# Optimization experiments

Hardware: AMD Instinct MI355X
Metric: run time of the kernel (lower is better)

Reference implementation:

```python
import jax, jax.numpy as jnp
import numpy as np

D_K = 64

def setup_inputs() -> dict:
    key = jax.random.key(0)
    kq, kk, kv, km = jax.random.split(key, 4)
    B, H, S, D = 8, 12, 1024, D_K
    Q = jax.random.normal(kq, (B, H, S, D), dtype=jnp.float32)
    K = jax.random.normal(kk, (B, H, S, D), dtype=jnp.float32)
    V = jax.random.normal(kv, (B, H, S, D), dtype=jnp.float32)
    # boolean mask: True = masked out (as used by masked_fill_)
    attn_mask = jax.random.randint(km, (B, H, S, S), 0, 2) == 1
    return {"Q": Q, "K": K, "V": V, "attn_mask": attn_mask}

def reference(Q, K, V, attn_mask):
    # scores: [B, H, S, S]
    scale = 1.0 / np.sqrt(D_K).astype(np.float32)
    scores = jnp.einsum('bhqd,bhkd->bhqk', Q, K) * scale
    scores = jnp.where(attn_mask, jnp.float32(-1e9), scores)
    attn = jax.nn.softmax(scores, axis=-1)
    context = jnp.einsum('bhqk,bhkd->bhqd', attn, V)
    return (context, attn)
```

## Files before the change

### kernel.cpp

```cpp
#include <hip/hip_runtime.h>

#define S_LEN  1024
#define D_KK   64
#define N_HEAD 96

#define TK 256
#define BQ 16

__global__ __launch_bounds__(256, 2) void attn_softmax_kernel(
    const float* __restrict__ Qg, const float* __restrict__ Kg,
    const int* __restrict__ maskg, float* __restrict__ attng)
{
    __shared__ float kt[D_KK][TK + 1];
    __shared__ float qs[BQ][68];

    const int t    = threadIdx.x;
    const int lane = t & 63;
    const int wave = t >> 6;
    const int head = blockIdx.y;
    const int q0   = blockIdx.x * BQ;
    const int rbase = wave << 2;

    {
        const int r  = t >> 4;
        const int d0 = (t & 15) << 2;
        const float4 qv = *(const float4*)(Qg + ((size_t)head * S_LEN + q0 + r) * D_KK + d0);
        qs[r][d0 + 0] = qv.x; qs[r][d0 + 1] = qv.y;
        qs[r][d0 + 2] = qv.z; qs[r][d0 + 3] = qv.w;
    }

    float s[4][16];

    for (int kt_i = 0; kt_i < S_LEN / TK; ++kt_i) {
        __syncthreads();
        {
            const int d0 = (t & 15) << 2;
            const int kb = t >> 4;
            #pragma unroll
            for (int c = 0; c < TK / 16; ++c) {
                const int kl = c * 16 + kb;
                const float4 kv = *(const float4*)(Kg + ((size_t)head * S_LEN + kt_i * TK + kl) * D_KK + d0);
                kt[d0 + 0][kl] = kv.x;
                kt[d0 + 1][kl] = kv.y;
                kt[d0 + 2][kl] = kv.z;
                kt[d0 + 3][kl] = kv.w;
            }
        }
        __syncthreads();

        float acc[4][4] = {{0.f,0.f,0.f,0.f},{0.f,0.f,0.f,0.f},
                           {0.f,0.f,0.f,0.f},{0.f,0.f,0.f,0.f}};
        for (int d0 = 0; d0 < D_KK; d0 += 4) {
            float4 qv[4];
            #pragma unroll
            for (int r = 0; r < 4; ++r)
                qv[r] = *(const float4*)(&qs[rbase + r][d0]);
            #pragma unroll
            for (int dd = 0; dd < 4; ++dd) {
                float kv[4];
                #pragma unroll
                for (int j = 0; j < 4; ++j)
                    kv[j] = kt[d0 + dd][lane + 64 * j];
                #pragma unroll
                for (int r = 0; r < 4; ++r) {
                    const float qd = (&qv[r].x)[dd];
                    #pragma unroll
                    for (int j = 0; j < 4; ++j)
                        acc[r][j] = fmaf(qd, kv[j], acc[r][j]);
                }
            }
        }
        #pragma unroll
        for (int r = 0; r < 4; ++r)
            #pragma unroll
            for (int j = 0; j < 4; ++j)
                s[r][kt_i * 4 + j] = acc[r][j] * 0.125f;
    }

    #pragma unroll
    for (int r = 0; r < 4; ++r) {
        const int q = q0 + rbase + r;
        const int*  mrow = maskg + ((size_t)head * S_LEN + q) * S_LEN;
        float*      arow = attng + ((size_t)head * S_LEN + q) * S_LEN;
        float m = -3.0e38f;
        #pragma unroll
        for (int j = 0; j < 16; ++j) {
            if (mrow[lane + 64 * j]) s[r][j] = -1.0e9f;
            m = fmaxf(m, s[r][j]);
        }
        #pragma unroll
        for (int off = 32; off >= 1; off >>= 1)
            m = fmaxf(m, __shfl_xor(m, off, 64));
        float l = 0.0f;
        #pragma unroll
        for (int j = 0; j < 16; ++j) {
            s[r][j] = __expf(s[r][j] - m);
            l += s[r][j];
        }
        #pragma unroll
        for (int off = 32; off >= 1; off >>= 1)
            l += __shfl_xor(l, off, 64);
        const float inv = 1.0f / l;
        #pragma unroll
        for (int j = 0; j < 16; ++j)
            arow[lane + 64 * j] = s[r][j] * inv;
    }
}

#define TKB 128

__global__ __launch_bounds__(256, 2) void attn_pv_kernel(
    const float* __restrict__ attng, const float* __restrict__ Vg,
    float* __restrict__ ctxg)
{
    __shared__ float at[64][132];
    __shared__ float vt[TKB][68];

    const int t    = threadIdx.x;
    const int tx   = t & 15;
    const int ty   = t >> 4;
    const int head = blockIdx.y;
    const int q0   = blockIdx.x * 64;

    float acc[4][4] = {{0.f,0.f,0.f,0.f},{0.f,0.f,0.f,0.f},
                       {0.f,0.f,0.f,0.f},{0.f,0.f,0.f,0.f}};

    for (int k0 = 0; k0 < S_LEN; k0 += TKB) {
        __syncthreads();
        #pragma unroll
        for (int p = 0; p < 8; ++p) {
            const int i  = t + 256 * p;
            const int q  = i >> 5;
            const int kk = (i & 31) << 2;
            const float4 a = *(const float4*)(attng + ((size_t)head * S_LEN + q0 + q) * S_LEN + k0 + kk);
            *(float4*)(&at[q][kk]) = a;
        }
        #pragma unroll
        for (int p = 0; p < 8; ++p) {
            const int i  = t + 256 * p;
            const int k  = i >> 4;
            const int d0 = (i & 15) << 2;
            const float4 v = *(const float4*)(Vg + ((size_t)head * S_LEN + k0 + k) * D_KK + d0);
            *(float4*)(&vt[k][d0]) = v;
        }
        __syncthreads();

        for (int k = 0; k < TKB; ++k) {
            const float4 v = *(const float4*)(&vt[k][tx << 2]);
            #pragma unroll
            for (int qq = 0; qq < 4; ++qq) {
                const float a = at[(ty << 2) + qq][k];
                acc[qq][0] = fmaf(a, v.x, acc[qq][0]);
                acc[qq][1] = fmaf(a, v.y, acc[qq][1]);
                acc[qq][2] = fmaf(a, v.z, acc[qq][2]);
                acc[qq][3] = fmaf(a, v.w, acc[qq][3]);
            }
        }
    }

    #pragma unroll
    for (int qq = 0; qq < 4; ++qq) {
        float4 o;
        o.x = acc[qq][0]; o.y = acc[qq][1]; o.z = acc[qq][2]; o.w = acc[qq][3];
        *(float4*)(ctxg + ((size_t)head * S_LEN + q0 + (ty << 2) + qq) * D_KK + (tx << 2)) = o;
    }
}

extern "C" void kernel_launch(void* const* d_in, const int* in_sizes, int n_in,
                              void* d_out, int out_size, void* d_ws, size_t ws_size,
                              hipStream_t stream) {
    const float* Q    = (const float*)d_in[0];
    const float* K    = (const float*)d_in[1];
    const float* V    = (const float*)d_in[2];
    const int*   mask = (const int*)d_in[3];

    float* ctx  = (float*)d_out;
    float* attn = ctx + (size_t)N_HEAD * S_LEN * D_KK;

    dim3 gridA(S_LEN / BQ, N_HEAD);
    attn_softmax_kernel<<<gridA, 256, 0, stream>>>(Q, K, mask, attn);

    dim3 gridB(S_LEN / 64, N_HEAD);
    attn_pv_kernel<<<gridB, 256, 0, stream>>>(attn, V, ctx);
}
```

Baseline: 1.041 ms.

## Fuse QK softmax and PV into one bf16 MFMA kernel

Replaces the two fp32 SIMT kernels with a single kernel that converts Q, K and V to bf16 and computes QK^T and PV with 16x16x32 bf16 MFMA instructions. Unnormalized exponentials are kept packed in registers, row sums are reduced, and the normalized probabilities are written to the attention output and reused directly for the PV product. This avoids re-reading the attention matrix from global memory. The softmax drops max subtraction, which risks overflow for large scores, and bf16 rounding lowers precision of both outputs. Holding 128 registers of packed probabilities per thread may also limit occupancy.

```diff
diff --git a/kernel.cpp b/kernel.cpp
--- a/kernel.cpp
+++ b/kernel.cpp
@@ -4,166 +4,169 @@
 #define D_KK   64
 #define N_HEAD 96
 
-#define TK 256
-#define BQ 16
+typedef float f32x4 __attribute__((ext_vector_type(4)));
+typedef short bf16x8 __attribute__((ext_vector_type(8)));
+typedef short bf16x4 __attribute__((ext_vector_type(4)));
 
-__global__ __launch_bounds__(256, 2) void attn_softmax_kernel(
+__device__ __forceinline__ unsigned short f2bf(float f) {
+    union { float f; unsigned u; } v; v.f = f;
+    unsigned r = v.u + 0x7fffu + ((v.u >> 16) & 1u);
+    return (unsigned short)(r >> 16);
+}
+__device__ __forceinline__ float bf2f(unsigned short b) {
+    union { float f; unsigned u; } v; v.u = ((unsigned)b) << 16;
+    return v.f;
+}
+
+__global__ __launch_bounds__(256, 2) void fused_attn_kernel(
     const float* __restrict__ Qg, const float* __restrict__ Kg,
-    const int* __restrict__ maskg, float* __restrict__ attng)
+    const float* __restrict__ Vg, const int* __restrict__ maskg,
+    float* __restrict__ ctxg, float* __restrict__ attng)
 {
-    __shared__ float kt[D_KK][TK + 1];
-    __shared__ float qs[BQ][68];
+    __shared__ short qs[64][72];
+    __shared__ short ks[128][72];
+    __shared__ short vt[64][136];
+    __shared__ short ps[64][136];
 
     const int t    = threadIdx.x;
     const int lane = t & 63;
     const int wave = t >> 6;
+    const int quad = lane >> 4;
+    const int l16  = lane & 15;
     const int head = blockIdx.y;
-    const int q0   = blockIdx.x * BQ;
-    const int rbase = wave << 2;
+    const int q0   = blockIdx.x * 64;
 
-    {
-        const int r  = t >> 4;
-        const int d0 = (t & 15) << 2;
-        const float4 qv = *(const float4*)(Qg + ((size_t)head * S_LEN + q0 + r) * D_KK + d0);
-        qs[r][d0 + 0] = qv.x; qs[r][d0 + 1] = qv.y;
-        qs[r][d0 + 2] = qv.z; qs[r][d0 + 3] = qv.w;
+    const size_t headQ = (size_t)head * S_LEN * D_KK;
+    const float* Qh = Qg + headQ + (size_t)q0 * D_KK;
+    const float* Kh = Kg + headQ;
+    const float* Vh = Vg + headQ;
+    const int*   mh = maskg + ((size_t)head * S_LEN + q0) * S_LEN;
+    float*       ah = attng + ((size_t)head * S_LEN + q0) * S_LEN;
+    float*       ch = ctxg + headQ + (size_t)q0 * D_KK;
+
+    #pragma unroll
+    for (int p = 0; p < 4; ++p) {
+        const int i = t + 256 * p;
+        const int row = i >> 4, c4 = (i & 15) << 2;
+        const f32x4 qv = *(const f32x4*)(Qh + (size_t)row * D_KK + c4);
+        bf16x4 qb;
+        qb[0] = (short)f2bf(qv[0]); qb[1] = (short)f2bf(qv[1]);
+        qb[2] = (short)f2bf(qv[2]); qb[3] = (short)f2bf(qv[3]);
+        *(bf16x4*)(&qs[row][c4]) = qb;
     }
+    __syncthreads();
 
-    float s[4][16];
+    bf16x8 aq[2];
+    #pragma unroll
+    for (int d0 = 0; d0 < 2; ++d0)
+        aq[d0] = *(const bf16x8*)(&qs[16 * wave + l16][d0 * 32 + quad * 8]);
 
-    for (int kt_i = 0; kt_i < S_LEN / TK; ++kt_i) {
+    unsigned pk[128];
+    float lsum[4] = {0.f, 0.f, 0.f, 0.f};
+
+    #pragma unroll
+    for (int kt = 0; kt < 8; ++kt) {
+        #pragma unroll
+        for (int p = 0; p < 8; ++p) {
+            const int i = t + 256 * p;
+            const int row = i >> 4, c4 = (i & 15) << 2;
+            const f32x4 kv = *(const f32x4*)(Kh + (size_t)(kt * 128 + row) * D_KK + c4);
+            bf16x4 kb;
+            kb[0] = (short)f2bf(kv[0]); kb[1] = (short)f2bf(kv[1]);
+            kb[2] = (short)f2bf(kv[2]); kb[3] = (short)f2bf(kv[3]);
+            *(bf16x4*)(&ks[row][c4]) = kb;
+        }
         __syncthreads();
-        {
-            const int d0 = (t & 15) << 2;
-            const int kb = t >> 4;
+
+        #pragma unroll
+        for (int ct = 0; ct < 8; ++ct) {
+            f32x4 c = {0.f, 0.f, 0.f, 0.f};
             #pragma unroll
-            for (int c = 0; c < TK / 16; ++c) {
-                const int kl = c * 16 + kb;
-                const float4 kv = *(const float4*)(Kg + ((size_t)head * S_LEN + kt_i * TK + kl) * D_KK + d0);
-                kt[d0 + 0][kl] = kv.x;
-                kt[d0 + 1][kl] = kv.y;
-                kt[d0 + 2][kl] = kv.z;
-                kt[d0 + 3][kl] = kv.w;
+            for (int d0 = 0; d0 < 2; ++d0) {
+                const bf16x8 b = *(const bf16x8*)(&ks[ct * 16 + l16][d0 * 32 + quad * 8]);
+                c = __builtin_amdgcn_mfma_f32_16x16x32_bf16(aq[d0], b, c, 0, 0, 0);
+            }
+            const int col = kt * 128 + ct * 16 + l16;
+            #pragma unroll
+            for (int r = 0; r < 4; ++r) {
+                const int row = 16 * wave + quad * 4 + r;
+                const int m = mh[(size_t)row * S_LEN + col];
+                const float pv = m ? 0.0f : __expf(c[r] * 0.125f);
+                lsum[r] += pv;
+                const unsigned pb = f2bf(pv);
+                const int pidx = ((kt * 8 + ct) << 1) + (r >> 1);
+                if ((r & 1) == 0) pk[pidx] = pb;
+                else              pk[pidx] |= pb << 16;
             }
         }
         __syncthreads();
-
-        float acc[4][4] = {{0.f,0.f,0.f,0.f},{0.f,0.f,0.f,0.f},
-                           {0.f,0.f,0.f,0.f},{0.f,0.f,0.f,0.f}};
-        for (int d0 = 0; d0 < D_KK; d0 += 4) {
-            float4 qv[4];
-            #pragma unroll
-            for (int r = 0; r < 4; ++r)
-                qv[r] = *(const float4*)(&qs[rbase + r][d0]);
-            #pragma unroll
-            for (int dd = 0; dd < 4; ++dd) {
-                float kv[4];
-                #pragma unroll
-                for (int j = 0; j < 4; ++j)
-                    kv[j] = kt[d0 + dd][lane + 64 * j];
-                #pragma unroll
-                for (int r = 0; r < 4; ++r) {
-                    const float qd = (&qv[r].x)[dd];
-                    #pragma unroll
-                    for (int j = 0; j < 4; ++j)
-                        acc[r][j] = fmaf(qd, kv[j], acc[r][j]);
-                }
-            }
-        }
-        #pragma unroll
-        for (int r = 0; r < 4; ++r)
-            #pragma unroll
-            for (int j = 0; j < 4; ++j)
-                s[r][kt_i * 4 + j] = acc[r][j] * 0.125f;
     }
 
     #pragma unroll
     for (int r = 0; r < 4; ++r) {
-        const int q = q0 + rbase + r;
-        const int*  mrow = maskg + ((size_t)head * S_LEN + q) * S_LEN;
-        float*      arow = attng + ((size_t)head * S_LEN + q) * S_LEN;
-        float m = -3.0e38f;
-        #pragma unroll
-        for (int j = 0; j < 16; ++j) {
-            if (mrow[lane + 64 * j]) s[r][j] = -1.0e9f;
-            m = fmaxf(m, s[r][j]);
-        }
-        #pragma unroll
-        for (int off = 32; off >= 1; off >>= 1)
-            m = fmaxf(m, __shfl_xor(m, off, 64));
-        float l = 0.0f;
-        #pragma unroll
-        for (int j = 0; j < 16; ++j) {
-            s[r][j] = __expf(s[r][j] - m);
-            l += s[r][j];
-        }
-        #pragma unroll
-        for (int off = 32; off >= 1; off >>= 1)
-            l += __shfl_xor(l, off, 64);
-        const float inv = 1.0f / l;
-        #pragma unroll
-        for (int j = 0; j < 16; ++j)
-            arow[lane + 64 * j] = s[r][j] * inv;
+        float v = lsum[r];
+        v += __shfl_xor(v, 1, 64);
+        v += __shfl_xor(v, 2, 64);
+        v += __shfl_xor(v, 4, 64);
+        v += __shfl_xor(v, 8, 64);
+        lsum[r] = 1.0f / v;
     }
-}
 
-#define TKB 128
+    f32x4 o[4];
+    #pragma unroll
+    for (int dt = 0; dt < 4; ++dt) o[dt] = (f32x4){0.f, 0.f, 0.f, 0.f};
 
-__global__ __launch_bounds__(256, 2) void attn_pv_kernel(
-    const float* __restrict__ attng, const float* __restrict__ Vg,
-    float* __restrict__ ctxg)
-{
-    __shared__ float at[64][132];
-    __shared__ float vt[TKB][68];
-
-    const int t    = threadIdx.x;
-    const int tx   = t & 15;
-    const int ty   = t >> 4;
-    const int head = blockIdx.y;
-    const int q0   = blockIdx.x * 64;
-
-    float acc[4][4] = {{0.f,0.f,0.f,0.f},{0.f,0.f,0.f,0.f},
-                       {0.f,0.f,0.f,0.f},{0.f,0.f,0.f,0.f}};
-
-    for (int k0 = 0; k0 < S_LEN; k0 += TKB) {
+    #pragma unroll
+    for (int kt = 0; kt < 8; ++kt) {
         __syncthreads();
         #pragma unroll
         for (int p = 0; p < 8; ++p) {
-            const int i  = t + 256 * p;
-            const int q  = i >> 5;
-            const int kk = (i & 31) << 2;
-            const float4 a = *(const float4*)(attng + ((size_t)head * S_LEN + q0 + q) * S_LEN + k0 + kk);
-            *(float4*)(&at[q][kk]) = a;
+            const int i = t + 256 * p;
+            const int k = i >> 4, d4 = (i & 15) << 2;
+            const f32x4 vv = *(const f32x4*)(Vh + (size_t)(kt * 128 + k) * D_KK + d4);
+            vt[d4 + 0][k] = (short)f2bf(vv[0]);
+            vt[d4 + 1][k] = (short)f2bf(vv[1]);
+            vt[d4 + 2][k] = (short)f2bf(vv[2]);
+            vt[d4 + 3][k] = (short)f2bf(vv[3]);
         }
         #pragma unroll
-        for (int p = 0; p < 8; ++p) {
-            const int i  = t + 256 * p;
-            const int k  = i >> 4;
-            const int d0 = (i & 15) << 2;
-            const float4 v = *(const float4*)(Vg + ((size_t)head * S_LEN + k0 + k) * D_KK + d0);
-            *(float4*)(&vt[k][d0]) = v;
+        for (int ct = 0; ct < 8; ++ct) {
+            #pragma unroll
+            for (int r = 0; r < 4; ++r) {
+                const int pidx = ((kt * 8 + ct) << 1) + (r >> 1);
+                const unsigned short pb = (r & 1) ? (unsigned short)(pk[pidx] >> 16)
+                                                  : (unsigned short)(pk[pidx] & 0xffffu);
+                const float pv = bf2f(pb) * lsum[r];
+                ps[16 * wave + quad * 4 + r][ct * 16 + l16] = (short)f2bf(pv);
+            }
         }
         __syncthreads();
-
-        for (int k = 0; k < TKB; ++k) {
-            const float4 v = *(const float4*)(&vt[k][tx << 2]);
+        #pragma unroll
+        for (int p = 0; p < 8; ++p) {
+            const int i = t + 256 * p;
+            const int row = i >> 5, c4 = (i & 31) << 2;
+            const bf16x4 pb4 = *(const bf16x4*)(&ps[row][c4]);
+            f32x4 av;
+            av[0] = bf2f((unsigned short)pb4[0]); av[1] = bf2f((unsigned short)pb4[1]);
+            av[2] = bf2f((unsigned short)pb4[2]); av[3] = bf2f((unsigned short)pb4[3]);
+            *(f32x4*)(ah + (size_t)row * S_LEN + kt * 128 + c4) = av;
+        }
+        #pragma unroll
+        for (int ks_ = 0; ks_ < 4; ++ks_) {
+            const bf16x8 a = *(const bf16x8*)(&ps[16 * wave + l16][ks_ * 32 + quad * 8]);
             #pragma unroll
-            for (int qq = 0; qq < 4; ++qq) {
-                const float a = at[(ty << 2) + qq][k];
-                acc[qq][0] = fmaf(a, v.x, acc[qq][0]);
-                acc[qq][1] = fmaf(a, v.y, acc[qq][1]);
-                acc[qq][2] = fmaf(a, v.z, acc[qq][2]);
-                acc[qq][3] = fmaf(a, v.w, acc[qq][3]);
+            for (int dt = 0; dt < 4; ++dt) {
+                const bf16x8 b = *(const bf16x8*)(&vt[dt * 16 + l16][ks_ * 32 + quad * 8]);
+                o[dt] = __builtin_amdgcn_mfma_f32_16x16x32_bf16(a, b, o[dt], 0, 0, 0);
             }
         }
     }
 
     #pragma unroll
-    for (int qq = 0; qq < 4; ++qq) {
-        float4 o;
-        o.x = acc[qq][0]; o.y = acc[qq][1]; o.z = acc[qq][2]; o.w = acc[qq][3];
-        *(float4*)(ctxg + ((size_t)head * S_LEN + q0 + (ty << 2) + qq) * D_KK + (tx << 2)) = o;
-    }
+    for (int dt = 0; dt < 4; ++dt)
+        #pragma unroll
+        for (int r = 0; r < 4; ++r)
+            ch[(size_t)(16 * wave + quad * 4 + r) * D_KK + dt * 16 + l16] = o[dt][r];
 }
 
 extern "C" void kernel_launch(void* const* d_in, const int* in_sizes, int n_in,
@@ -177,9 +180,6 @@
     float* ctx  = (float*)d_out;
     float* attn = ctx + (size_t)N_HEAD * S_LEN * D_KK;
 
-    dim3 gridA(S_LEN / BQ, N_HEAD);
-    attn_softmax_kernel<<<gridA, 256, 0, stream>>>(Q, K, mask, attn);
-
-    dim3 gridB(S_LEN / 64, N_HEAD);
-    attn_pv_kernel<<<gridB, 256, 0, stream>>>(attn, V, ctx);
+    dim3 grid(S_LEN / 64, N_HEAD);
+    fused_attn_kernel<<<grid, 256, 0, stream>>>(Q, K, V, mask, ctx, attn);
 }
```

Result: slower. 1.306 ms (+25.5%).
